# Performance work log

Hardware: AMD Instinct MI355X
Metric: run time of the kernel (lower is better)

Reference implementation:

```python
import jax, jax.numpy as jnp
import numpy as np

SEQ, D_IN, D_OUT = 8192, 1024, 1024

def setup_inputs() -> dict:
    key = jax.random.key(0)
    kx, kq, kk, kv = jax.random.split(key, 4)
    scale = 1.0 / np.sqrt(D_IN)
    return {
        "x": jax.random.normal(kx, (SEQ, D_IN), dtype=jnp.float32),
        "Wq": jax.random.normal(kq, (D_OUT, D_IN), dtype=jnp.float32) * scale,
        "Wk": jax.random.normal(kk, (D_OUT, D_IN), dtype=jnp.float32) * scale,
        "Wv": jax.random.normal(kv, (D_OUT, D_IN), dtype=jnp.float32) * scale,
    }

def reference(x, Wq, Wk, Wv):
    # nn.Linear: y = x @ W.T (no bias)
    q = x @ Wq.T            # [S, d_out]
    k = x @ Wk.T            # [S, d_out]
    v = x @ Wv.T            # [S, d_out]
    d_k = k.shape[-1]
    scores = (q @ k.T) / jnp.sqrt(jnp.float32(d_k))   # [S, S]
    attn = jax.nn.softmax(scores, axis=-1)
    return attn @ v         # [S, d_out]
```

## Files before the change

kernel.cpp:

```cpp
#include <hip/hip_runtime.h>

typedef unsigned short ushort_t;
typedef __attribute__((ext_vector_type(8))) __bf16 bf16x8;
typedef __attribute__((ext_vector_type(4))) float f32x4;

#define SEQ 8192
#define DIN 1024
#define DOUT 1024

#define OM_BF16 0
#define OM_F32  1
#define OM_EXP  2
#define OM_NORM 3

__device__ __forceinline__ ushort_t f2bf(float f) {
  union { float f; unsigned u; } c; c.f = f;
  unsigned u = c.u;
  return (ushort_t)((u + 0x7fffu + ((u >> 16) & 1u)) >> 16);
}

__device__ __forceinline__ void async16(ushort_t* lds, const ushort_t* g) {
  __builtin_amdgcn_global_load_lds(
      (__attribute__((address_space(1))) void*)g,
      (__attribute__((address_space(3))) void*)lds, 16, 0, 0);
}

__global__ __launch_bounds__(256) void cvt_all_kernel(
    const float* __restrict__ x, const float* __restrict__ wq,
    const float* __restrict__ wk, const float* __restrict__ wv,
    ushort_t* __restrict__ xb, ushort_t* __restrict__ wqkb,
    ushort_t* __restrict__ wvb) {
  int b = blockIdx.x;
  const float* src;
  ushort_t* dst;
  int idx;
  if (b < 8192) {
    src = x; dst = xb; idx = b * 256 + threadIdx.x;
  } else {
    int r = b - 8192;
    int w = r >> 10;
    idx = (r & 1023) * 256 + threadIdx.x;
    if (w == 0)      { src = wq; dst = wqkb; }
    else if (w == 1) { src = wk; dst = wqkb + DOUT * DIN; }
    else             { src = wv; dst = wvb; }
  }
  float4 f = ((const float4*)src)[idx];
  ushort4 o;
  o.x = f2bf(f.x); o.y = f2bf(f.y); o.z = f2bf(f.z); o.w = f2bf(f.w);
  ((ushort4*)dst)[idx] = o;
}

__global__ __launch_bounds__(256) void rowsum_inv_kernel(const float* __restrict__ rsp,
                                                         float* __restrict__ invrs) {
  int r = blockIdx.x * 256 + threadIdx.x;
  float s = 0.f;
  #pragma unroll
  for (int p2 = 0; p2 < 64; ++p2) s += rsp[p2 * SEQ + r];
  invrs[r] = 1.0f / s;
}

template <int OUTMODE, int SWZ, int BK>
__global__ __launch_bounds__(256) void gemm_bt(const ushort_t* __restrict__ A,
                                               const ushort_t* __restrict__ B,
                                               void* __restrict__ C,
                                               int lda, int ldb, int ldc,
                                               int K, float scale,
                                               float* __restrict__ rsp,
                                               const float* __restrict__ invrs) {
  constexpr int CPR = BK / 8;
  constexpr int NI = BK / 16;
  __shared__ ushort_t As[128 * BK];
  __shared__ ushort_t Bs[128 * BK];
  const int t = threadIdx.x;
  const int lane = t & 63;
  const int wave = t >> 6;
  const int wr = wave >> 1, wc = wave & 1;
  const int quad = lane >> 4, r16 = lane & 15;

  int mt, nt;
  if (SWZ == 1) {
    mt = blockIdx.x * (gridDim.y >> 3) + (blockIdx.y >> 3);
    nt = blockIdx.y & 7;
  } else {
    mt = blockIdx.y;
    nt = blockIdx.x;
  }
  const int rowBase = mt * 128;
  const int colBase = nt * 128;

  unsigned offA[NI], offB[NI];
  #pragma unroll
  for (int i = 0; i < NI; ++i) {
    int c = t + i * 256;
    int row = c / CPR;
    int kq = c & (CPR - 1);
    int kqs = (kq & ~7) | ((kq & 7) ^ (row & 7));
    offA[i] = (unsigned)((rowBase + row) * lda + kqs * 8);
    offB[i] = (unsigned)((colBase + row) * ldb + kqs * 8);
  }

  f32x4 acc[4][4] = {};

  const int nk = K / BK;
  for (int kt = 0; kt < nk; ++kt) {
    #pragma unroll
    for (int i = 0; i < NI; ++i) {
      async16(&As[(t + i * 256) * 8], A + offA[i]); offA[i] += BK;
      async16(&Bs[(t + i * 256) * 8], B + offB[i]); offB[i] += BK;
    }
    __syncthreads();
    #pragma unroll
    for (int ks = 0; ks < BK / 32; ++ks) {
      bf16x8 af[4], bfr[4];
      #pragma unroll
      for (int mi = 0; mi < 4; ++mi) {
        int row = wr * 64 + mi * 16 + r16;
        int kq = ks * 4 + quad;
        int c = row * CPR + ((kq & ~7) | ((kq & 7) ^ (row & 7)));
        af[mi] = *(const bf16x8*)&As[c * 8];
      }
      #pragma unroll
      for (int ni = 0; ni < 4; ++ni) {
        int row = wc * 64 + ni * 16 + r16;
        int kq = ks * 4 + quad;
        int c = row * CPR + ((kq & ~7) | ((kq & 7) ^ (row & 7)));
        bfr[ni] = *(const bf16x8*)&Bs[c * 8];
      }
      #pragma unroll
      for (int mi = 0; mi < 4; ++mi)
        #pragma unroll
        for (int ni = 0; ni < 4; ++ni)
          acc[mi][ni] = __builtin_amdgcn_mfma_f32_16x16x32_bf16(af[mi], bfr[ni],
                                                                acc[mi][ni], 0, 0, 0);
    }
    __syncthreads();
  }

  float iv[4][4];
  if (OUTMODE == OM_NORM) {
    #pragma unroll
    for (int mi = 0; mi < 4; ++mi)
      #pragma unroll
      for (int r = 0; r < 4; ++r)
        iv[mi][r] = invrs[rowBase + wr * 64 + mi * 16 + quad * 4 + r];
  }

  float psum[4][4];
  if (OUTMODE == OM_EXP) {
    #pragma unroll
    for (int mi = 0; mi < 4; ++mi)
      #pragma unroll
      for (int r = 0; r < 4; ++r) psum[mi][r] = 0.f;
  }

  #pragma unroll
  for (int mi = 0; mi < 4; ++mi)
    #pragma unroll
    for (int ni = 0; ni < 4; ++ni)
      #pragma unroll
      for (int r = 0; r < 4; ++r) {
        int grow = rowBase + wr * 64 + mi * 16 + quad * 4 + r;
        int gcol = colBase + wc * 64 + ni * 16 + r16;
        float a = acc[mi][ni][r];
        if (OUTMODE == OM_F32) {
          ((float*)C)[(size_t)grow * ldc + gcol] = a * scale;
        } else if (OUTMODE == OM_BF16) {
          ((ushort_t*)C)[(size_t)grow * ldc + gcol] = f2bf(a * scale);
        } else if (OUTMODE == OM_EXP) {
          float e = exp2f(a * scale);
          psum[mi][r] += e;
          ((ushort_t*)C)[(size_t)grow * ldc + gcol] = f2bf(e);
        } else {
          ((float*)C)[(size_t)grow * ldc + gcol] = a * iv[mi][r];
        }
      }

  if (OUTMODE == OM_EXP) {
    float* lds_rs = (float*)As;
    #pragma unroll
    for (int mi = 0; mi < 4; ++mi)
      #pragma unroll
      for (int r = 0; r < 4; ++r) {
        float s = psum[mi][r];
        s += __shfl_xor(s, 1, 64);
        s += __shfl_xor(s, 2, 64);
        s += __shfl_xor(s, 4, 64);
        s += __shfl_xor(s, 8, 64);
        if (r16 == 0)
          lds_rs[wc * 128 + wr * 64 + mi * 16 + quad * 4 + r] = s;
      }
    __syncthreads();
    if (t < 128)
      rsp[(size_t)nt * SEQ + rowBase + t] = lds_rs[t] + lds_rs[128 + t];
  }
}

extern "C" void kernel_launch(void* const* d_in, const int* in_sizes, int n_in,
                              void* d_out, int out_size, void* d_ws, size_t ws_size,
                              hipStream_t stream) {
  const float* x  = (const float*)d_in[0];
  const float* Wq = (const float*)d_in[1];
  const float* Wk = (const float*)d_in[2];
  const float* Wv = (const float*)d_in[3];
  float* out = (float*)d_out;

  char* p = (char*)d_ws;
  ushort_t* xb   = (ushort_t*)p; p += (size_t)SEQ * DIN * 2;
  ushort_t* wqkb = (ushort_t*)p; p += (size_t)2 * DOUT * DIN * 2;
  ushort_t* wvb  = (ushort_t*)p; p += (size_t)DOUT * DIN * 2;
  ushort_t* qkb  = (ushort_t*)p; p += (size_t)SEQ * 2 * DOUT * 2;
  ushort_t* vtb  = (ushort_t*)p; p += (size_t)DOUT * SEQ * 2;
  float*    rsp  = (float*)p;    p += (size_t)64 * SEQ * 4;
  float*    irs  = (float*)p;    p += (size_t)SEQ * 4;
  ushort_t* Sb   = (ushort_t*)p; p += (size_t)SEQ * SEQ * 2;

  cvt_all_kernel<<<8192 + 3 * 1024, 256, 0, stream>>>(x, Wq, Wk, Wv, xb, wqkb, wvb);

  dim3 blk(256);
  gemm_bt<OM_BF16, 0, 64><<<dim3(2048 / 128, SEQ / 128), blk, 0, stream>>>(
      xb, wqkb, qkb, DIN, DIN, 2 * DOUT, DIN, 1.0f, nullptr, nullptr);

  gemm_bt<OM_BF16, 0, 128><<<dim3(SEQ / 128, DOUT / 128), blk, 0, stream>>>(
      wvb, xb, vtb, DIN, DIN, SEQ, DIN, 1.0f, nullptr, nullptr);

  gemm_bt<OM_EXP, 0, 64><<<dim3(SEQ / 128, SEQ / 128), blk, 0, stream>>>(
      qkb, qkb + DOUT, Sb, 2 * DOUT, 2 * DOUT, SEQ, DIN,
      0.03125f * 1.44269504f, rsp, nullptr);

  rowsum_inv_kernel<<<SEQ / 256, blk, 0, stream>>>(rsp, irs);

  gemm_bt<OM_NORM, 1, 128><<<dim3(DOUT / 128, SEQ / 128), blk, 0, stream>>>(
      Sb, vtb, out, SEQ, SEQ, DOUT, SEQ, 1.0f, nullptr, irs);
}
```

Measured before the change: 496.8 us.

## Replace 128x128 GEMM with 256-row tiles and a 4-stage async LDS pipeline

Rewrites the shared GEMM kernel to use 512-thread blocks with 256xBN output tiles, BK=32 k-slices, and a 4-buffer async global-to-LDS pipeline driven by explicit vmcnt waits, so loads overlap the MFMA work. It also adds a grouped block-id remap for L2 locality, a new XOR swizzle for LDS, and s_setprio around the MFMA loop. Larger tiles raise arithmetic intensity but use more registers and LDS (about 96KB per block), which limits occupancy. The partial row-sum count drops from 64 to 32 to match the wider S tiles.

Result: faster. 475.1 us (-4.4%).

```diff
diff --git a/kernel.cpp b/kernel.cpp
--- a/kernel.cpp
+++ b/kernel.cpp
@@ -9,7 +9,6 @@
 #define DOUT 1024
 
 #define OM_BF16 0
-#define OM_F32  1
 #define OM_EXP  2
 #define OM_NORM 3
 
@@ -24,6 +23,13 @@
       (__attribute__((address_space(1))) void*)g,
       (__attribute__((address_space(3))) void*)lds, 16, 0, 0);
 }
+
+template <int N>
+__device__ __forceinline__ void waitv() {
+  asm volatile("s_waitcnt vmcnt(%0)" :: "n"(N) : "memory");
+}
+
+__device__ __forceinline__ int fsw(int row) { return (row ^ (row >> 2)) & 3; }
 
 __global__ __launch_bounds__(256) void cvt_all_kernel(
     const float* __restrict__ x, const float* __restrict__ wq,
@@ -55,118 +61,146 @@
   int r = blockIdx.x * 256 + threadIdx.x;
   float s = 0.f;
   #pragma unroll
-  for (int p2 = 0; p2 < 64; ++p2) s += rsp[p2 * SEQ + r];
+  for (int p2 = 0; p2 < 32; ++p2) s += rsp[p2 * SEQ + r];
   invrs[r] = 1.0f / s;
 }
 
-template <int OUTMODE, int SWZ, int BK>
-__global__ __launch_bounds__(256) void gemm_bt(const ushort_t* __restrict__ A,
-                                               const ushort_t* __restrict__ B,
-                                               void* __restrict__ C,
-                                               int lda, int ldb, int ldc,
-                                               int K, float scale,
-                                               float* __restrict__ rsp,
-                                               const float* __restrict__ invrs) {
-  constexpr int CPR = BK / 8;
-  constexpr int NI = BK / 16;
-  __shared__ ushort_t As[128 * BK];
-  __shared__ ushort_t Bs[128 * BK];
+template <int OUTMODE, int BN>
+__global__ __launch_bounds__(512, 2) void gemm256(
+    const ushort_t* __restrict__ A, const ushort_t* __restrict__ B,
+    void* __restrict__ C, int lda, int ldb, int ldc, int K, float scale,
+    float* __restrict__ rsp, const float* __restrict__ invrs) {
+  constexpr int BKS = 32;
+  constexpr int NIN = BN / 64;
+  constexpr int NA = 2;
+  constexpr int NB = BN * 4 / 512;
+  constexpr int LPG = NA + NB;
+  constexpr int AST = 256 * BKS;
+  constexpr int BST = BN * BKS;
+  __shared__ ushort_t As[4 * AST];
+  __shared__ ushort_t Bs[4 * BST];
+
   const int t = threadIdx.x;
   const int lane = t & 63;
   const int wave = t >> 6;
-  const int wr = wave >> 1, wc = wave & 1;
+  const int wr = wave >> 2, wc = wave & 3;
   const int quad = lane >> 4, r16 = lane & 15;
 
-  int mt, nt;
-  if (SWZ == 1) {
-    mt = blockIdx.x * (gridDim.y >> 3) + (blockIdx.y >> 3);
-    nt = blockIdx.y & 7;
-  } else {
-    mt = blockIdx.y;
-    nt = blockIdx.x;
-  }
-  const int rowBase = mt * 128;
-  const int colBase = nt * 128;
-
-  unsigned offA[NI], offB[NI];
-  #pragma unroll
-  for (int i = 0; i < NI; ++i) {
-    int c = t + i * 256;
-    int row = c / CPR;
-    int kq = c & (CPR - 1);
-    int kqs = (kq & ~7) | ((kq & 7) ^ (row & 7));
-    offA[i] = (unsigned)((rowBase + row) * lda + kqs * 8);
-    offB[i] = (unsigned)((colBase + row) * ldb + kqs * 8);
-  }
-
-  f32x4 acc[4][4] = {};
-
-  const int nk = K / BK;
-  for (int kt = 0; kt < nk; ++kt) {
-    #pragma unroll
-    for (int i = 0; i < NI; ++i) {
-      async16(&As[(t + i * 256) * 8], A + offA[i]); offA[i] += BK;
-      async16(&Bs[(t + i * 256) * 8], B + offB[i]); offB[i] += BK;
-    }
-    __syncthreads();
-    #pragma unroll
-    for (int ks = 0; ks < BK / 32; ++ks) {
-      bf16x8 af[4], bfr[4];
-      #pragma unroll
-      for (int mi = 0; mi < 4; ++mi) {
-        int row = wr * 64 + mi * 16 + r16;
-        int kq = ks * 4 + quad;
-        int c = row * CPR + ((kq & ~7) | ((kq & 7) ^ (row & 7)));
-        af[mi] = *(const bf16x8*)&As[c * 8];
-      }
-      #pragma unroll
-      for (int ni = 0; ni < 4; ++ni) {
-        int row = wc * 64 + ni * 16 + r16;
-        int kq = ks * 4 + quad;
-        int c = row * CPR + ((kq & ~7) | ((kq & 7) ^ (row & 7)));
-        bfr[ni] = *(const bf16x8*)&Bs[c * 8];
-      }
-      #pragma unroll
-      for (int mi = 0; mi < 4; ++mi)
-        #pragma unroll
-        for (int ni = 0; ni < 4; ++ni)
-          acc[mi][ni] = __builtin_amdgcn_mfma_f32_16x16x32_bf16(af[mi], bfr[ni],
-                                                                acc[mi][ni], 0, 0, 0);
-    }
-    __syncthreads();
-  }
-
-  float iv[4][4];
-  if (OUTMODE == OM_NORM) {
-    #pragma unroll
-    for (int mi = 0; mi < 4; ++mi)
+  const int gx = gridDim.x;
+  const int nwg = gx * gridDim.y;
+  const int bid = blockIdx.y * gx + blockIdx.x;
+  const int q8 = nwg >> 3;
+  const int b2 = (bid & 7) * q8 + (bid >> 3);
+  const int mt = b2 / gx;
+  const int nt = b2 - mt * gx;
+  const int rowBase = mt * 256;
+  const int colBase = nt * BN;
+
+  unsigned offA[NA], offB[NB];
+  #pragma unroll
+  for (int i = 0; i < NA; ++i) {
+    int c = t + i * 512, row = c >> 2, sl = c & 3;
+    offA[i] = (unsigned)((rowBase + row) * lda + ((sl ^ fsw(row)) << 3));
+  }
+  #pragma unroll
+  for (int i = 0; i < NB; ++i) {
+    int c = t + i * 512, row = c >> 2, sl = c & 3;
+    offB[i] = (unsigned)((colBase + row) * ldb + ((sl ^ fsw(row)) << 3));
+  }
+
+  f32x4 acc[8][NIN] = {};
+
+  const int NS = K / BKS;
+
+  #pragma unroll
+  for (int s = 0; s < 3; ++s) {
+    #pragma unroll
+    for (int i = 0; i < NA; ++i) {
+      async16(&As[s * AST + (t + i * 512) * 8], A + offA[i]); offA[i] += BKS;
+    }
+    #pragma unroll
+    for (int i = 0; i < NB; ++i) {
+      async16(&Bs[s * BST + (t + i * 512) * 8], B + offB[i]); offB[i] += BKS;
+    }
+  }
+
+  for (int s = 0; s < NS; ++s) {
+    const int rem = NS - 1 - s;
+    if (rem >= 2)      waitv<2 * LPG>();
+    else if (rem == 1) waitv<LPG>();
+    else               waitv<0>();
+    __builtin_amdgcn_s_barrier();
+    asm volatile("" ::: "memory");
+    __builtin_amdgcn_sched_barrier(0);
+
+    const ushort_t* as = &As[(s & 3) * AST];
+    const ushort_t* bs = &Bs[(s & 3) * BST];
+    bf16x8 af[8], bfr[NIN];
+    #pragma unroll
+    for (int mi = 0; mi < 8; ++mi) {
+      int row = wr * 128 + mi * 16 + r16;
+      int sl = quad ^ fsw(row);
+      af[mi] = *(const bf16x8*)&as[(row * 4 + sl) * 8];
+    }
+    #pragma unroll
+    for (int ni = 0; ni < NIN; ++ni) {
+      int row = wc * (BN / 4) + ni * 16 + r16;
+      int sl = quad ^ fsw(row);
+      bfr[ni] = *(const bf16x8*)&bs[(row * 4 + sl) * 8];
+    }
+
+    if (s + 3 < NS) {
+      const int sb = (s + 3) & 3;
+      #pragma unroll
+      for (int i = 0; i < NA; ++i) {
+        async16(&As[sb * AST + (t + i * 512) * 8], A + offA[i]); offA[i] += BKS;
+      }
+      #pragma unroll
+      for (int i = 0; i < NB; ++i) {
+        async16(&Bs[sb * BST + (t + i * 512) * 8], B + offB[i]); offB[i] += BKS;
+      }
+    }
+
+    __builtin_amdgcn_s_setprio(1);
+    #pragma unroll
+    for (int mi = 0; mi < 8; ++mi)
+      #pragma unroll
+      for (int ni = 0; ni < NIN; ++ni)
+        acc[mi][ni] = __builtin_amdgcn_mfma_f32_16x16x32_bf16(af[mi], bfr[ni],
+                                                              acc[mi][ni], 0, 0, 0);
+    __builtin_amdgcn_s_setprio(0);
+    __builtin_amdgcn_sched_barrier(0);
+  }
+
+  float iv[8][4];
+  if constexpr (OUTMODE == OM_NORM) {
+    #pragma unroll
+    for (int mi = 0; mi < 8; ++mi)
       #pragma unroll
       for (int r = 0; r < 4; ++r)
-        iv[mi][r] = invrs[rowBase + wr * 64 + mi * 16 + quad * 4 + r];
-  }
-
-  float psum[4][4];
-  if (OUTMODE == OM_EXP) {
-    #pragma unroll
-    for (int mi = 0; mi < 4; ++mi)
+        iv[mi][r] = invrs[rowBase + wr * 128 + mi * 16 + quad * 4 + r];
+  }
+
+  float psum[8][4];
+  if constexpr (OUTMODE == OM_EXP) {
+    #pragma unroll
+    for (int mi = 0; mi < 8; ++mi)
       #pragma unroll
       for (int r = 0; r < 4; ++r) psum[mi][r] = 0.f;
   }
 
   #pragma unroll
-  for (int mi = 0; mi < 4; ++mi)
-    #pragma unroll
-    for (int ni = 0; ni < 4; ++ni)
+  for (int mi = 0; mi < 8; ++mi)
+    #pragma unroll
+    for (int ni = 0; ni < NIN; ++ni)
       #pragma unroll
       for (int r = 0; r < 4; ++r) {
-        int grow = rowBase + wr * 64 + mi * 16 + quad * 4 + r;
-        int gcol = colBase + wc * 64 + ni * 16 + r16;
+        int grow = rowBase + wr * 128 + mi * 16 + quad * 4 + r;
+        int gcol = colBase + wc * (BN / 4) + ni * 16 + r16;
         float a = acc[mi][ni][r];
-        if (OUTMODE == OM_F32) {
-          ((float*)C)[(size_t)grow * ldc + gcol] = a * scale;
-        } else if (OUTMODE == OM_BF16) {
+        if constexpr (OUTMODE == OM_BF16) {
           ((ushort_t*)C)[(size_t)grow * ldc + gcol] = f2bf(a * scale);
-        } else if (OUTMODE == OM_EXP) {
+        } else if constexpr (OUTMODE == OM_EXP) {
           float e = exp2f(a * scale);
           psum[mi][r] += e;
           ((ushort_t*)C)[(size_t)grow * ldc + gcol] = f2bf(e);
@@ -175,23 +209,25 @@
         }
       }
 
-  if (OUTMODE == OM_EXP) {
+  if constexpr (OUTMODE == OM_EXP) {
+    __syncthreads();
     float* lds_rs = (float*)As;
     #pragma unroll
-    for (int mi = 0; mi < 4; ++mi)
+    for (int mi = 0; mi < 8; ++mi)
       #pragma unroll
       for (int r = 0; r < 4; ++r) {
-        float s = psum[mi][r];
-        s += __shfl_xor(s, 1, 64);
-        s += __shfl_xor(s, 2, 64);
-        s += __shfl_xor(s, 4, 64);
-        s += __shfl_xor(s, 8, 64);
+        float sv = psum[mi][r];
+        sv += __shfl_xor(sv, 1, 64);
+        sv += __shfl_xor(sv, 2, 64);
+        sv += __shfl_xor(sv, 4, 64);
+        sv += __shfl_xor(sv, 8, 64);
         if (r16 == 0)
-          lds_rs[wc * 128 + wr * 64 + mi * 16 + quad * 4 + r] = s;
+          lds_rs[wc * 256 + wr * 128 + mi * 16 + quad * 4 + r] = sv;
       }
     __syncthreads();
-    if (t < 128)
-      rsp[(size_t)nt * SEQ + rowBase + t] = lds_rs[t] + lds_rs[128 + t];
+    if (t < 256)
+      rsp[(size_t)nt * SEQ + rowBase + t] =
+          lds_rs[t] + lds_rs[256 + t] + lds_rs[512 + t] + lds_rs[768 + t];
   }
 }
 
@@ -216,19 +252,19 @@
 
   cvt_all_kernel<<<8192 + 3 * 1024, 256, 0, stream>>>(x, Wq, Wk, Wv, xb, wqkb, wvb);
 
-  dim3 blk(256);
-  gemm_bt<OM_BF16, 0, 64><<<dim3(2048 / 128, SEQ / 128), blk, 0, stream>>>(
+  dim3 blk(512);
+  gemm256<OM_BF16, 256><<<dim3(2048 / 256, SEQ / 256), blk, 0, stream>>>(
       xb, wqkb, qkb, DIN, DIN, 2 * DOUT, DIN, 1.0f, nullptr, nullptr);
 
-  gemm_bt<OM_BF16, 0, 128><<<dim3(SEQ / 128, DOUT / 128), blk, 0, stream>>>(
+  gemm256<OM_BF16, 128><<<dim3(SEQ / 128, DOUT / 256), blk, 0, stream>>>(
       wvb, xb, vtb, DIN, DIN, SEQ, DIN, 1.0f, nullptr, nullptr);
 
-  gemm_bt<OM_EXP, 0, 64><<<dim3(SEQ / 128, SEQ / 128), blk, 0, stream>>>(
+  gemm256<OM_EXP, 256><<<dim3(SEQ / 256, SEQ / 256), blk, 0, stream>>>(
       qkb, qkb + DOUT, Sb, 2 * DOUT, 2 * DOUT, SEQ, DIN,
       0.03125f * 1.44269504f, rsp, nullptr);
 
-  rowsum_inv_kernel<<<SEQ / 256, blk, 0, stream>>>(rsp, irs);
-
-  gemm_bt<OM_NORM, 1, 128><<<dim3(DOUT / 128, SEQ / 128), blk, 0, stream>>>(
+  rowsum_inv_kernel<<<SEQ / 256, 256, 0, stream>>>(rsp, irs);
+
+  gemm256<OM_NORM, 128><<<dim3(DOUT / 128, SEQ / 256), blk, 0, stream>>>(
       Sb, vtb, out, SEQ, SEQ, DOUT, SEQ, 1.0f, nullptr, irs);
 }
```
